# Kernel optimization log

Hardware: AMD Instinct MI355X
Metric: run time of the kernel (lower is better)

## Reference

```python
import jax, jax.numpy as jnp
import numpy as np

# dims: M scalars (0e), K vectors (1e) in input; T = tp_features; N = batch of atoms
M, K, T, N = 128, 64, 64, 131072
D_IN = M + 3 * K  # 320, e3nn layout: [128x0e | 64x1e flattened as (mul, 3)]


def _act_norm(f):
    # e3nn Activation normalizes act so E_{z~N(0,1)}[act(z)^2] = 1
    z = np.linspace(-8.0, 8.0, 20001)
    pdf = np.exp(-0.5 * z * z) / np.sqrt(2.0 * np.pi)
    return float(np.sqrt(np.trapz(f(z) ** 2 * pdf, z)))

C_SILU = _act_norm(lambda z: z / (1.0 + np.exp(-z)))
C_RELU = _act_norm(lambda z: np.maximum(z, 0.0))
INV_SQRT_M = float(1.0 / np.sqrt(M))
INV_SQRT_K = float(1.0 / np.sqrt(K))
INV_SQRT_3 = float(1.0 / np.sqrt(3.0))  # wigner_3j(1,1,0) = delta_ij/sqrt(3)
TP_NORM = float(1.0 / np.sqrt(2.0 * T * T))  # fan-in over the 2 paths into 0e


def setup_inputs() -> dict:
    key = jax.random.key(0)
    ks = jax.random.split(key, 11)
    f32 = jnp.float32
    return {
        "x": jax.random.normal(ks[0], (N, D_IN), f32),
        "input_shift": jnp.zeros((D_IN,), f32),
        "output_scale": jnp.ones((), f32),
        # PerceptronLayer 1: Linear (Mx0e+Kx1e) -> ((M+K)x0e + Kx1e)
        "w0_1": jax.random.normal(ks[1], (M, M + K), f32),
        "b0_1": jnp.zeros((M + K,), f32),
        "w1_1": jax.random.normal(ks[2], (K, K), f32),
        # PerceptronLayer 2 (same irreps, resnet applies)
        "w0_2": jax.random.normal(ks[3], (M, M + K), f32),
        "b0_2": jnp.zeros((M + K,), f32),
        "w1_2": jax.random.normal(ks[4], (K, K), f32),
        # linear_out: (Mx0e+Kx1e) -> (Tx0e+Tx1e)
        "w0_o": jax.random.normal(ks[5], (M, T), f32),
        "b0_o": jnp.zeros((T,), f32),
        "w1_o": jax.random.normal(ks[6], (K, T), f32),
        # FullyConnectedTensorProduct (tp, tp) -> 1x0e: paths 0e*0e->0e, 1e*1e->0e
        "w_tp0": jax.random.normal(ks[7], (T, T), f32),
        "w_tp1": jax.random.normal(ks[8], (T, T), f32),
    }


def _linear(xs, xv, w0, b0, w1):
    # e3nn o3.Linear: per-irrep dense mixing with 1/sqrt(fan_in), bias on 0e only
    ys = xs @ w0 * INV_SQRT_M + b0          # [N, M+K] scalars + gates
    yv = jnp.einsum('nki,kj->nji', xv, w1) * INV_SQRT_K  # [N, K, 3]
    return ys, yv


def _gate(ys, yv):
    # e3nn Gate: silu on 0e scalars, relu on 0e gates, gate the 1e vectors
    s = jax.nn.silu(ys[:, :M]) / C_SILU     # [N, M]
    g = jax.nn.relu(ys[:, M:]) / C_RELU     # [N, K]
    return s, yv * g[:, :, None]


def reference(x, input_shift, output_scale,
              w0_1, b0_1, w1_1, w0_2, b0_2, w1_2,
              w0_o, b0_o, w1_o, w_tp0, w_tp1):
    x = x - input_shift
    xs = x[:, :M]                           # [N, M] 0e block
    xv = x[:, M:].reshape(-1, K, 3)         # [N, K, 3] 1e block
    for (w0, b0, w1) in ((w0_1, b0_1, w1_1), (w0_2, b0_2, w1_2)):
        ys, yv = _linear(xs, xv, w0, b0, w1)
        s, v = _gate(ys, yv)
        xs = xs + s                         # resnet: irreps_in == irreps_out
        xv = xv + v
    # linear_out -> irreps_tp = Tx0e + Tx1e
    zs = xs @ w0_o * INV_SQRT_M + b0_o                    # [N, T]
    zv = jnp.einsum('nki,kj->nji', xv, w1_o) * INV_SQRT_K # [N, T, 3]
    # FullyConnectedTensorProduct(z, z) -> 0e (avoid [N,T,T] blowup)
    y0 = jnp.sum((zs @ w_tp0) * zs, axis=-1)                                    # [N]
    y1 = jnp.sum(jnp.einsum('nui,uv->nvi', zv, w_tp1) * zv, axis=(1, 2)) * INV_SQRT_3
    y = (y0 + y1) * TP_NORM / output_scale
    return y[:, None]
```

## Files before the change

kernel.cpp:

```cpp
#include <hip/hip_runtime.h>
#include <math.h>


typedef _Float16 f16;
typedef _Float16 f16x8 __attribute__((ext_vector_type(8)));
typedef __fp16   fp16x2 __attribute__((ext_vector_type(2)));
typedef float    f32x4 __attribute__((ext_vector_type(4)));
typedef int      i32x4 __attribute__((ext_vector_type(4)));

#define MFMA16(a, b, c) __builtin_amdgcn_mfma_f32_16x16x32_f16(a, b, c, 0, 0, 0)

constexpr float INV_SQRT_M = 0.08838834764831845f;
constexpr float INV_SQRT_K = 0.125f;
constexpr float INV_SQRT_3 = 0.57735026918962576f;
constexpr float TP_NORM    = 0.011048543456039806f;

#define OFF_W01 0
#define OFF_W11 24576
#define OFF_W02 28672
#define OFF_W12 53248
#define OFF_W0O 57344
#define OFF_W1O 65536
#define OFF_TP0 69632
#define OFF_TP1 73728
#define PACK_UNITS 9728
#define FB01 38912
#define FB02 39104
#define FB0O 39296
#define TOTAL_UNITS (PACK_UNITS + 448)

#define LDS_W1     24576
#define LDS_BIAS_F 14336
#define LDS_W0O    0
#define LDS_W1O    8192
#define LDS_TP0    12288
#define LDS_TP1    16384
#define LDS_B0O_F  10240

#define NTHR 512

__global__ void pack_and_consts(const float* __restrict__ w01, const float* __restrict__ w11,
                                const float* __restrict__ w02, const float* __restrict__ w12,
                                const float* __restrict__ w0o, const float* __restrict__ w1o,
                                const float* __restrict__ tp0, const float* __restrict__ tp1,
                                const float* __restrict__ b01, const float* __restrict__ b02,
                                const float* __restrict__ b0o,
                                f16* __restrict__ dst, float* __restrict__ ws) {
    if (blockIdx.x == 40) {
        __shared__ double red[256];
        const int t = threadIdx.x;
        double acc_s = 0.0, acc_r = 0.0;
        for (int i = t; i <= 20000; i += 256) {
            const double z = -8.0 + (16.0 * (double)i) / 20000.0;
            const double pdf = exp(-0.5 * z * z) / 2.5066282746310002;
            const double sil = z / (1.0 + exp(-z));
            const double wgt = (i == 0 || i == 20000) ? 0.5 : 1.0;
            acc_s += wgt * sil * sil * pdf;
            if (z > 0.0) acc_r += wgt * z * z * pdf;
        }
        red[t] = acc_s;
        __syncthreads();
        for (int o = 128; o > 0; o >>= 1) { if (t < o) red[t] += red[t + o]; __syncthreads(); }
        const double tot_s = red[0];
        __syncthreads();
        red[t] = acc_r;
        __syncthreads();
        for (int o = 128; o > 0; o >>= 1) { if (t < o) red[t] += red[t + o]; __syncthreads(); }
        if (t == 0) {
            const double dz = 16.0 / 20000.0;
            ws[0] = (float)(1.0 / sqrt(tot_s * dz));
            ws[1] = (float)(1.0 / sqrt(red[0] * dz));
        }
        return;
    }
    int u = blockIdx.x * 256 + threadIdx.x;
    if (u >= TOTAL_UNITS) return;
    if (u >= PACK_UNITS) {
        const int idx = u - PACK_UNITS;
        float* dstF = (float*)dst;
        if (idx < 192)      dstF[FB01 + idx] = b01[idx];
        else if (idx < 384) dstF[FB02 + (idx - 192)] = b02[idx - 192];
        else                dstF[FB0O + (idx - 384)] = b0o[idx - 384];
        return;
    }
    const float* src; int NC, base, lu = u; float sc;
    if      (lu < 3072) {            src = w01; NC = 192; base = OFF_W01; sc = INV_SQRT_M; }
    else if (lu < 3584) { lu -= 3072; src = w11; NC = 64;  base = OFF_W11; sc = INV_SQRT_K; }
    else if (lu < 6656) { lu -= 3584; src = w02; NC = 192; base = OFF_W02; sc = INV_SQRT_M; }
    else if (lu < 7168) { lu -= 6656; src = w12; NC = 64;  base = OFF_W12; sc = INV_SQRT_K; }
    else if (lu < 8192) { lu -= 7168; src = w0o; NC = 64;  base = OFF_W0O; sc = INV_SQRT_M; }
    else if (lu < 8704) { lu -= 8192; src = w1o; NC = 64;  base = OFF_W1O; sc = INV_SQRT_K; }
    else if (lu < 9216) { lu -= 8704; src = tp0; NC = 64;  base = OFF_TP0; sc = 1.0f; }
    else                { lu -= 9216; src = tp1; NC = 64;  base = OFF_TP1; sc = INV_SQRT_3; }
    const int lane = lu & 63;
    const int frag = lu >> 6;
    const int NT = NC >> 4;
    const int kstep = frag / NT, nj = frag - kstep * NT;
    const int gl  = lane >> 4;
    const int col = nj * 16 + (lane & 15);
    f16 tmp[8];
    #pragma unroll
    for (int e = 0; e < 8; ++e) {
        const int row = kstep * 32 + ((e >> 2) << 4) + (gl << 2) + (e & 3);
        tmp[e] = (f16)(src[(size_t)row * NC + col] * sc);
    }
    *(f16x8*)&dst[(size_t)(base) + (size_t)lu * 8] = *(f16x8*)tmp;
}

__device__ __forceinline__ int pk2i(float a, float b) {
    union { fp16x2 h; int i; } u;
    u.h = __builtin_amdgcn_cvt_pkrtz(a, b);
    return u.i;
}

__device__ __forceinline__ f16x8 packB(f32x4 t0, f32x4 t1) {
    union { i32x4 i; f16x8 v; } u;
    u.i[0] = pk2i(t0[0], t0[1]);
    u.i[1] = pk2i(t0[2], t0[3]);
    u.i[2] = pk2i(t1[0], t1[1]);
    u.i[3] = pk2i(t1[2], t1[3]);
    return u.v;
}

union Frag { f16x8 v; fp16x2 h2[4]; };

__device__ __forceinline__ void resblock32(
    Frag (&xsS)[2][4], Frag (&xvS)[2][3][2],
    const f16* lds, float invCS, float invCR, int l, int g)
{
    const float* biasF = (const float*)lds + LDS_BIAS_F;

    f16x8 xsB[2][4];
    #pragma unroll
    for (int h = 0; h < 2; ++h)
        #pragma unroll
        for (int ks = 0; ks < 4; ++ks)
            xsB[h][ks] = xsS[h][ks].v;

    f16x8 aP[4];
    #pragma unroll
    for (int ks = 0; ks < 4; ++ks)
        aP[ks] = *(const f16x8*)&lds[(size_t)(ks * 12 * 64 + l) * 8];
    f32x4 biasP = *(const f32x4*)&biasF[g * 4];

    float gate[2][4][4];
    #pragma unroll
    for (int nj = 0; nj < 12; ++nj) {
        f16x8 aC[4];
        #pragma unroll
        for (int ks = 0; ks < 4; ++ks) aC[ks] = aP[ks];
        const f32x4 bias = biasP;
        if (nj < 11) {
            #pragma unroll
            for (int ks = 0; ks < 4; ++ks)
                aP[ks] = *(const f16x8*)&lds[(size_t)((ks * 12 + nj + 1) * 64 + l) * 8];
            biasP = *(const f32x4*)&biasF[(nj + 1) * 16 + g * 4];
        }
        f32x4 acc0 = {0.f, 0.f, 0.f, 0.f}, acc1 = {0.f, 0.f, 0.f, 0.f};
        #pragma unroll
        for (int ks = 0; ks < 4; ++ks) {
            acc0 = MFMA16(aC[ks], xsB[0][ks], acc0);
            acc1 = MFMA16(aC[ks], xsB[1][ks], acc1);
        }
        #pragma unroll
        for (int h = 0; h < 2; ++h) {
            const f32x4 acc = h ? acc1 : acc0;
            if (nj < 8) {
                float s[4];
                #pragma unroll
                for (int r = 0; r < 4; ++r) {
                    const float ys = acc[r] + bias[r];
                    s[r] = ys * __builtin_amdgcn_rcpf(1.0f + __expf(-ys)) * invCS;
                }
                xsS[h][nj >> 1].h2[2 * (nj & 1)]     += __builtin_amdgcn_cvt_pkrtz(s[0], s[1]);
                xsS[h][nj >> 1].h2[2 * (nj & 1) + 1] += __builtin_amdgcn_cvt_pkrtz(s[2], s[3]);
            } else {
                #pragma unroll
                for (int r = 0; r < 4; ++r) {
                    const float ys = acc[r] + bias[r];
                    gate[h][nj - 8][r] = fmaxf(ys, 0.f) * invCR;
                }
            }
        }
    }

    #pragma unroll
    for (int i = 0; i < 3; ++i) {
        f32x4 av[2][4];
        #pragma unroll
        for (int nj = 0; nj < 4; ++nj) {
            f32x4 a0 = {0.f, 0.f, 0.f, 0.f}, a1 = {0.f, 0.f, 0.f, 0.f};
            #pragma unroll
            for (int ks = 0; ks < 2; ++ks) {
                const f16x8 a = *(const f16x8*)&lds[LDS_W1 + (size_t)((ks * 4 + nj) * 64 + l) * 8];
                a0 = MFMA16(a, xvS[0][i][ks].v, a0);
                a1 = MFMA16(a, xvS[1][i][ks].v, a1);
            }
            av[0][nj] = a0;
            av[1][nj] = a1;
        }
        #pragma unroll
        for (int nj = 0; nj < 4; ++nj)
            #pragma unroll
            for (int h = 0; h < 2; ++h) {
                float u[4];
                #pragma unroll
                for (int r = 0; r < 4; ++r)
                    u[r] = av[h][nj][r] * gate[h][nj][r];
                xvS[h][i][nj >> 1].h2[2 * (nj & 1)]     += __builtin_amdgcn_cvt_pkrtz(u[0], u[1]);
                xvS[h][i][nj >> 1].h2[2 * (nj & 1) + 1] += __builtin_amdgcn_cvt_pkrtz(u[2], u[3]);
            }
    }
}

__global__ __launch_bounds__(NTHR, 2)
void corrnet_lds(const float* __restrict__ x, const float* __restrict__ shift,
                 const float* __restrict__ oscale,
                 const f16* __restrict__ wp, const float* __restrict__ consts,
                 float* __restrict__ out)
{
    __shared__ __align__(16) f16 smem[29056];
    float* smemF = (float*)smem;
    const float* wpF = (const float*)wp;

    const int t = threadIdx.x;
    const int l = t & 63;
    const int g = l >> 4;
    const int c = l & 15;
    const size_t n0 = (size_t)blockIdx.x * 256 + (size_t)(t >> 6) * 32;

    const float invCS = consts[0], invCR = consts[1];
    const float inv_os = 1.0f / oscale[0];

    #pragma unroll
    for (int it = 0; it < 7; ++it) {
        const int u = it * NTHR + t;
        *(f16x8*)&smem[(size_t)u * 8] = *(const f16x8*)&wp[(size_t)u * 8];
    }
    if (t < 48)
        ((f32x4*)&smemF[LDS_BIAS_F])[t] = ((const f32x4*)&wpF[FB01])[t];

    Frag xsS[2][4];
    Frag xvS[2][3][2];
    #pragma unroll
    for (int h = 0; h < 2; ++h) {
        const float* xrow = x + (n0 + h * 16 + c) * 320;
        #pragma unroll
        for (int ks = 0; ks < 4; ++ks) {
            const int col = ks * 32 + g * 4;
            const f32x4 t0 = *(const f32x4*)(xrow + col)      - *(const f32x4*)(shift + col);
            const f32x4 t1 = *(const f32x4*)(xrow + col + 16) - *(const f32x4*)(shift + col + 16);
            xsS[h][ks].v = packB(t0, t1);
        }
        f32x4 tmp[3][4];
        #pragma unroll
        for (int tau = 0; tau < 4; ++tau) {
            const int col = 128 + 3 * (tau * 16 + g * 4);
            const f32x4 a0 = *(const f32x4*)(xrow + col)     - *(const f32x4*)(shift + col);
            const f32x4 a1 = *(const f32x4*)(xrow + col + 4) - *(const f32x4*)(shift + col + 4);
            const f32x4 a2 = *(const f32x4*)(xrow + col + 8) - *(const f32x4*)(shift + col + 8);
            float arr[12];
            #pragma unroll
            for (int e = 0; e < 4; ++e) {
                arr[e] = a0[e]; arr[4 + e] = a1[e]; arr[8 + e] = a2[e];
            }
            #pragma unroll
            for (int r = 0; r < 4; ++r)
                #pragma unroll
                for (int i = 0; i < 3; ++i)
                    tmp[i][tau][r] = arr[3 * r + i];
        }
        #pragma unroll
        for (int i = 0; i < 3; ++i)
            #pragma unroll
            for (int ks = 0; ks < 2; ++ks)
                xvS[h][i][ks].v = packB(tmp[i][2 * ks], tmp[i][2 * ks + 1]);
    }

    __syncthreads();
    resblock32(xsS, xvS, smem, invCS, invCR, l, g);
    __syncthreads();

    #pragma unroll
    for (int it = 0; it < 7; ++it) {
        const int u = it * NTHR + t;
        *(f16x8*)&smem[(size_t)u * 8] = *(const f16x8*)&wp[(size_t)(OFF_W02) + (size_t)u * 8];
    }
    if (t < 48)
        ((f32x4*)&smemF[LDS_BIAS_F])[t] = ((const f32x4*)&wpF[FB02])[t];
    __syncthreads();
    resblock32(xsS, xvS, smem, invCS, invCR, l, g);
    __syncthreads();

    #pragma unroll
    for (int it = 0; it < 5; ++it) {
        const int u = it * NTHR + t;
        *(f16x8*)&smem[(size_t)u * 8] = *(const f16x8*)&wp[(size_t)(OFF_W0O) + (size_t)u * 8];
    }
    if (t < 16)
        ((f32x4*)&smemF[LDS_B0O_F])[t] = ((const f32x4*)&wpF[FB0O])[t];
    __syncthreads();

    f32x4 zs[2][4];
    #pragma unroll
    for (int nj = 0; nj < 4; ++nj) {
        f32x4 acc0 = {0.f, 0.f, 0.f, 0.f}, acc1 = {0.f, 0.f, 0.f, 0.f};
        #pragma unroll
        for (int ks = 0; ks < 4; ++ks) {
            const f16x8 a = *(const f16x8*)&smem[LDS_W0O + (size_t)((ks * 4 + nj) * 64 + l) * 8];
            acc0 = MFMA16(a, xsS[0][ks].v, acc0);
            acc1 = MFMA16(a, xsS[1][ks].v, acc1);
        }
        const f32x4 bias = *(const f32x4*)&smemF[LDS_B0O_F + nj * 16 + g * 4];
        #pragma unroll
        for (int r = 0; r < 4; ++r) {
            zs[0][nj][r] = acc0[r] + bias[r];
            zs[1][nj][r] = acc1[r] + bias[r];
        }
    }

    float part[2]  = {0.f, 0.f};
    float part1[2] = {0.f, 0.f};

    {
        f16x8 zsB[2][2];
        #pragma unroll
        for (int h = 0; h < 2; ++h)
            #pragma unroll
            for (int ks = 0; ks < 2; ++ks)
                zsB[h][ks] = packB(zs[h][2 * ks], zs[h][2 * ks + 1]);
        #pragma unroll
        for (int nj = 0; nj < 4; ++nj) {
            f32x4 acc0 = {0.f, 0.f, 0.f, 0.f}, acc1 = {0.f, 0.f, 0.f, 0.f};
            #pragma unroll
            for (int ks = 0; ks < 2; ++ks) {
                const f16x8 a = *(const f16x8*)&smem[LDS_TP0 + (size_t)((ks * 4 + nj) * 64 + l) * 8];
                acc0 = MFMA16(a, zsB[0][ks], acc0);
                acc1 = MFMA16(a, zsB[1][ks], acc1);
            }
            #pragma unroll
            for (int r = 0; r < 4; ++r) {
                part[0] += acc0[r] * zs[0][nj][r];
                part[1] += acc1[r] * zs[1][nj][r];
            }
        }
    }

    #pragma unroll
    for (int i = 0; i < 3; ++i) {
        f32x4 zv[2][4];
        #pragma unroll
        for (int nj = 0; nj < 4; ++nj) {
            f32x4 acc0 = {0.f, 0.f, 0.f, 0.f}, acc1 = {0.f, 0.f, 0.f, 0.f};
            #pragma unroll
            for (int ks = 0; ks < 2; ++ks) {
                const f16x8 a = *(const f16x8*)&smem[LDS_W1O + (size_t)((ks * 4 + nj) * 64 + l) * 8];
                acc0 = MFMA16(a, xvS[0][i][ks].v, acc0);
                acc1 = MFMA16(a, xvS[1][i][ks].v, acc1);
            }
            #pragma unroll
            for (int r = 0; r < 4; ++r) {
                zv[0][nj][r] = acc0[r];
                zv[1][nj][r] = acc1[r];
            }
        }
        f16x8 zvB[2][2];
        #pragma unroll
        for (int h = 0; h < 2; ++h)
            #pragma unroll
            for (int ks = 0; ks < 2; ++ks)
                zvB[h][ks] = packB(zv[h][2 * ks], zv[h][2 * ks + 1]);
        #pragma unroll
        for (int nj = 0; nj < 4; ++nj) {
            f32x4 acc0 = {0.f, 0.f, 0.f, 0.f}, acc1 = {0.f, 0.f, 0.f, 0.f};
            #pragma unroll
            for (int ks = 0; ks < 2; ++ks) {
                const f16x8 a = *(const f16x8*)&smem[LDS_TP1 + (size_t)((ks * 4 + nj) * 64 + l) * 8];
                acc0 = MFMA16(a, zvB[0][ks], acc0);
                acc1 = MFMA16(a, zvB[1][ks], acc1);
            }
            #pragma unroll
            for (int r = 0; r < 4; ++r) {
                part1[0] += acc0[r] * zv[0][nj][r];
                part1[1] += acc1[r] * zv[1][nj][r];
            }
        }
    }
    #pragma unroll
    for (int h = 0; h < 2; ++h)
        part[h] += part1[h];

    #pragma unroll
    for (int h = 0; h < 2; ++h) {
        part[h] += __shfl_xor(part[h], 16, 64);
        part[h] += __shfl_xor(part[h], 32, 64);
    }

    if (l < 16)
        out[n0 + l] = part[0] * TP_NORM * inv_os;
    else if (l < 32)
        out[n0 + 16 + (l - 16)] = part[1] * TP_NORM * inv_os;
}

extern "C" void kernel_launch(void* const* d_in, const int* in_sizes, int n_in,
                              void* d_out, int out_size, void* d_ws, size_t ws_size,
                              hipStream_t stream) {
    const float* x      = (const float*)d_in[0];
    const float* shift  = (const float*)d_in[1];
    const float* oscale = (const float*)d_in[2];
    const float* w01    = (const float*)d_in[3];
    const float* b01    = (const float*)d_in[4];
    const float* w11    = (const float*)d_in[5];
    const float* w02    = (const float*)d_in[6];
    const float* b02    = (const float*)d_in[7];
    const float* w12    = (const float*)d_in[8];
    const float* w0o    = (const float*)d_in[9];
    const float* b0o    = (const float*)d_in[10];
    const float* w1o    = (const float*)d_in[11];
    const float* wtp0   = (const float*)d_in[12];
    const float* wtp1   = (const float*)d_in[13];
    float* out    = (float*)d_out;
    float* consts = (float*)d_ws;
    f16*   wp     = (f16*)((char*)d_ws + 16);

    pack_and_consts<<<41, 256, 0, stream>>>(
        w01, w11, w02, w12, w0o, w1o, wtp0, wtp1, b01, b02, b0o, wp, consts);

    const int nblocks = 131072 / 256;
    corrnet_lds<<<nblocks, NTHR, 0, stream>>>(
        x, shift, oscale, wp, consts, out);
}
```

Before: 80.15 us.

## Switch matrix multiplies from 16x16x32 to 32x32x16 MFMA tiles

Replaces every 16x16x32 f16 MFMA with the 32x32x16 variant, so each wave covers its 32 atoms with one 32-wide tile instead of two 16-wide halves. The weight packing, input fragment loading, bias indexing and output reduction are rewritten for the new register layout. The gate activations are now kept as packed half pairs and the vector update multiplies in half precision. The aim is fewer MFMA instructions and fewer LDS weight reads per atom, at the cost of larger accumulators, more register pressure and slightly lower precision in the gating step.

Result: slower. 87.07 us (+8.6%).

```diff
diff --git a/kernel.cpp b/kernel.cpp
--- a/kernel.cpp
+++ b/kernel.cpp
@@ -6,9 +6,10 @@
 typedef _Float16 f16x8 __attribute__((ext_vector_type(8)));
 typedef __fp16   fp16x2 __attribute__((ext_vector_type(2)));
 typedef float    f32x4 __attribute__((ext_vector_type(4)));
+typedef float    f32x16 __attribute__((ext_vector_type(16)));
 typedef int      i32x4 __attribute__((ext_vector_type(4)));
 
-#define MFMA16(a, b, c) __builtin_amdgcn_mfma_f32_16x16x32_f16(a, b, c, 0, 0, 0)
+#define MFMA32(a, b, c) __builtin_amdgcn_mfma_f32_32x32x16_f16(a, b, c, 0, 0, 0)
 
 constexpr float INV_SQRT_M = 0.08838834764831845f;
 constexpr float INV_SQRT_K = 0.125f;
@@ -83,25 +84,24 @@
         else                dstF[FB0O + (idx - 384)] = b0o[idx - 384];
         return;
     }
-    const float* src; int NC, base, lu = u; float sc;
-    if      (lu < 3072) {            src = w01; NC = 192; base = OFF_W01; sc = INV_SQRT_M; }
-    else if (lu < 3584) { lu -= 3072; src = w11; NC = 64;  base = OFF_W11; sc = INV_SQRT_K; }
-    else if (lu < 6656) { lu -= 3584; src = w02; NC = 192; base = OFF_W02; sc = INV_SQRT_M; }
-    else if (lu < 7168) { lu -= 6656; src = w12; NC = 64;  base = OFF_W12; sc = INV_SQRT_K; }
-    else if (lu < 8192) { lu -= 7168; src = w0o; NC = 64;  base = OFF_W0O; sc = INV_SQRT_M; }
-    else if (lu < 8704) { lu -= 8192; src = w1o; NC = 64;  base = OFF_W1O; sc = INV_SQRT_K; }
-    else if (lu < 9216) { lu -= 8704; src = tp0; NC = 64;  base = OFF_TP0; sc = 1.0f; }
-    else                { lu -= 9216; src = tp1; NC = 64;  base = OFF_TP1; sc = INV_SQRT_3; }
+    const float* src; int NC, NSTEP, base, lu = u; float sc;
+    if      (lu < 3072) {            src = w01; NC = 192; NSTEP = 8; base = OFF_W01; sc = INV_SQRT_M; }
+    else if (lu < 3584) { lu -= 3072; src = w11; NC = 64;  NSTEP = 4; base = OFF_W11; sc = INV_SQRT_K; }
+    else if (lu < 6656) { lu -= 3584; src = w02; NC = 192; NSTEP = 8; base = OFF_W02; sc = INV_SQRT_M; }
+    else if (lu < 7168) { lu -= 6656; src = w12; NC = 64;  NSTEP = 4; base = OFF_W12; sc = INV_SQRT_K; }
+    else if (lu < 8192) { lu -= 7168; src = w0o; NC = 64;  NSTEP = 8; base = OFF_W0O; sc = INV_SQRT_M; }
+    else if (lu < 8704) { lu -= 8192; src = w1o; NC = 64;  NSTEP = 4; base = OFF_W1O; sc = INV_SQRT_K; }
+    else if (lu < 9216) { lu -= 8704; src = tp0; NC = 64;  NSTEP = 4; base = OFF_TP0; sc = 1.0f; }
+    else                { lu -= 9216; src = tp1; NC = 64;  NSTEP = 4; base = OFF_TP1; sc = INV_SQRT_3; }
     const int lane = lu & 63;
     const int frag = lu >> 6;
-    const int NT = NC >> 4;
-    const int kstep = frag / NT, nj = frag - kstep * NT;
-    const int gl  = lane >> 4;
-    const int col = nj * 16 + (lane & 15);
+    const int oc = frag / NSTEP, s = frag - oc * NSTEP;
+    const int gl  = lane >> 5;
+    const int col = oc * 32 + (lane & 31);
     f16 tmp[8];
     #pragma unroll
     for (int e = 0; e < 8; ++e) {
-        const int row = kstep * 32 + ((e >> 2) << 4) + (gl << 2) + (e & 3);
+        const int row = s * 16 + (e & 3) + 8 * (e >> 2) + 4 * gl;
         tmp[e] = (f16)(src[(size_t)row * NC + col] * sc);
     }
     *(f16x8*)&dst[(size_t)(base) + (size_t)lu * 8] = *(f16x8*)tmp;
@@ -124,92 +124,80 @@
 
 union Frag { f16x8 v; fp16x2 h2[4]; };
 
-__device__ __forceinline__ void resblock32(
-    Frag (&xsS)[2][4], Frag (&xvS)[2][3][2],
-    const f16* lds, float invCS, float invCR, int l, int g)
+__device__ __forceinline__ f32x16 zero16() {
+    f32x16 z = {0.f,0.f,0.f,0.f,0.f,0.f,0.f,0.f,0.f,0.f,0.f,0.f,0.f,0.f,0.f,0.f};
+    return z;
+}
+
+__device__ __forceinline__ void resblock32x32(
+    Frag (&xsF)[8], Frag (&xvF)[3][4],
+    const f16* lds, float invCS, float invCR, int l, int hi)
 {
     const float* biasF = (const float*)lds + LDS_BIAS_F;
 
-    f16x8 xsB[2][4];
-    #pragma unroll
-    for (int h = 0; h < 2; ++h)
-        #pragma unroll
-        for (int ks = 0; ks < 4; ++ks)
-            xsB[h][ks] = xsS[h][ks].v;
-
-    f16x8 aP[4];
-    #pragma unroll
-    for (int ks = 0; ks < 4; ++ks)
-        aP[ks] = *(const f16x8*)&lds[(size_t)(ks * 12 * 64 + l) * 8];
-    f32x4 biasP = *(const f32x4*)&biasF[g * 4];
-
-    float gate[2][4][4];
-    #pragma unroll
-    for (int nj = 0; nj < 12; ++nj) {
-        f16x8 aC[4];
-        #pragma unroll
-        for (int ks = 0; ks < 4; ++ks) aC[ks] = aP[ks];
-        const f32x4 bias = biasP;
-        if (nj < 11) {
-            #pragma unroll
-            for (int ks = 0; ks < 4; ++ks)
-                aP[ks] = *(const f16x8*)&lds[(size_t)((ks * 12 + nj + 1) * 64 + l) * 8];
-            biasP = *(const f32x4*)&biasF[(nj + 1) * 16 + g * 4];
-        }
-        f32x4 acc0 = {0.f, 0.f, 0.f, 0.f}, acc1 = {0.f, 0.f, 0.f, 0.f};
-        #pragma unroll
-        for (int ks = 0; ks < 4; ++ks) {
-            acc0 = MFMA16(aC[ks], xsB[0][ks], acc0);
-            acc1 = MFMA16(aC[ks], xsB[1][ks], acc1);
-        }
-        #pragma unroll
-        for (int h = 0; h < 2; ++h) {
-            const f32x4 acc = h ? acc1 : acc0;
-            if (nj < 8) {
-                float s[4];
+    f16x8 xsB[8];
+    #pragma unroll
+    for (int s = 0; s < 8; ++s) xsB[s] = xsF[s].v;
+
+    fp16x2 gate[2][8];
+    #pragma unroll
+    for (int oc = 0; oc < 6; ++oc) {
+        f32x16 acc = zero16();
+        #pragma unroll
+        for (int sg = 0; sg < 8; ++sg) {
+            const f16x8 a = *(const f16x8*)&lds[(size_t)((oc * 8 + sg) * 64 + l) * 8];
+            acc = MFMA32(a, xsB[sg], acc);
+        }
+        float ysv[16];
+        #pragma unroll
+        for (int q = 0; q < 4; ++q) {
+            const f32x4 b4 = *(const f32x4*)&biasF[oc * 32 + 8 * q + 4 * hi];
+            #pragma unroll
+            for (int r2 = 0; r2 < 4; ++r2)
+                ysv[4 * q + r2] = acc[4 * q + r2] + b4[r2];
+        }
+        if (oc < 4) {
+            #pragma unroll
+            for (int s = 0; s < 2; ++s)
                 #pragma unroll
-                for (int r = 0; r < 4; ++r) {
-                    const float ys = acc[r] + bias[r];
-                    s[r] = ys * __builtin_amdgcn_rcpf(1.0f + __expf(-ys)) * invCS;
+                for (int d = 0; d < 4; ++d) {
+                    const float y0 = ysv[8 * s + 2 * d], y1 = ysv[8 * s + 2 * d + 1];
+                    const float s0 = y0 * __builtin_amdgcn_rcpf(1.0f + __expf(-y0)) * invCS;
+                    const float s1 = y1 * __builtin_amdgcn_rcpf(1.0f + __expf(-y1)) * invCS;
+                    xsF[2 * oc + s].h2[d] += __builtin_amdgcn_cvt_pkrtz(s0, s1);
                 }
-                xsS[h][nj >> 1].h2[2 * (nj & 1)]     += __builtin_amdgcn_cvt_pkrtz(s[0], s[1]);
-                xsS[h][nj >> 1].h2[2 * (nj & 1) + 1] += __builtin_amdgcn_cvt_pkrtz(s[2], s[3]);
-            } else {
+        } else {
+            #pragma unroll
+            for (int s = 0; s < 2; ++s)
                 #pragma unroll
-                for (int r = 0; r < 4; ++r) {
-                    const float ys = acc[r] + bias[r];
-                    gate[h][nj - 8][r] = fmaxf(ys, 0.f) * invCR;
-                }
-            }
+                for (int d = 0; d < 4; ++d)
+                    gate[oc - 4][4 * s + d] = __builtin_amdgcn_cvt_pkrtz(
+                        fmaxf(ysv[8 * s + 2 * d], 0.f) * invCR,
+                        fmaxf(ysv[8 * s + 2 * d + 1], 0.f) * invCR);
         }
     }
 
     #pragma unroll
     for (int i = 0; i < 3; ++i) {
-        f32x4 av[2][4];
-        #pragma unroll
-        for (int nj = 0; nj < 4; ++nj) {
-            f32x4 a0 = {0.f, 0.f, 0.f, 0.f}, a1 = {0.f, 0.f, 0.f, 0.f};
-            #pragma unroll
-            for (int ks = 0; ks < 2; ++ks) {
-                const f16x8 a = *(const f16x8*)&lds[LDS_W1 + (size_t)((ks * 4 + nj) * 64 + l) * 8];
-                a0 = MFMA16(a, xvS[0][i][ks].v, a0);
-                a1 = MFMA16(a, xvS[1][i][ks].v, a1);
-            }
-            av[0][nj] = a0;
-            av[1][nj] = a1;
-        }
-        #pragma unroll
-        for (int nj = 0; nj < 4; ++nj)
-            #pragma unroll
-            for (int h = 0; h < 2; ++h) {
-                float u[4];
+        f16x8 xvB4[4];
+        #pragma unroll
+        for (int sg = 0; sg < 4; ++sg) xvB4[sg] = xvF[i][sg].v;
+        #pragma unroll
+        for (int oc = 0; oc < 2; ++oc) {
+            f32x16 acc = zero16();
+            #pragma unroll
+            for (int sg = 0; sg < 4; ++sg) {
+                const f16x8 a = *(const f16x8*)&lds[LDS_W1 + (size_t)((oc * 4 + sg) * 64 + l) * 8];
+                acc = MFMA32(a, xvB4[sg], acc);
+            }
+            #pragma unroll
+            for (int s = 0; s < 2; ++s)
                 #pragma unroll
-                for (int r = 0; r < 4; ++r)
-                    u[r] = av[h][nj][r] * gate[h][nj][r];
-                xvS[h][i][nj >> 1].h2[2 * (nj & 1)]     += __builtin_amdgcn_cvt_pkrtz(u[0], u[1]);
-                xvS[h][i][nj >> 1].h2[2 * (nj & 1) + 1] += __builtin_amdgcn_cvt_pkrtz(u[2], u[3]);
-            }
+                for (int d = 0; d < 4; ++d)
+                    xvF[i][2 * oc + s].h2[d] +=
+                        __builtin_amdgcn_cvt_pkrtz(acc[8 * s + 2 * d], acc[8 * s + 2 * d + 1])
+                        * gate[oc][4 * s + d];
+        }
     }
 }
 
@@ -223,10 +211,10 @@
     float* smemF = (float*)smem;
     const float* wpF = (const float*)wp;
 
-    const int t = threadIdx.x;
-    const int l = t & 63;
-    const int g = l >> 4;
-    const int c = l & 15;
+    const int t  = threadIdx.x;
+    const int l  = t & 63;
+    const int hi = l >> 5;
+    const int c  = l & 31;
     const size_t n0 = (size_t)blockIdx.x * 256 + (size_t)(t >> 6) * 32;
 
     const float invCS = consts[0], invCR = consts[1];
@@ -240,45 +228,49 @@
     if (t < 48)
         ((f32x4*)&smemF[LDS_BIAS_F])[t] = ((const f32x4*)&wpF[FB01])[t];
 
-    Frag xsS[2][4];
-    Frag xvS[2][3][2];
-    #pragma unroll
-    for (int h = 0; h < 2; ++h) {
-        const float* xrow = x + (n0 + h * 16 + c) * 320;
-        #pragma unroll
-        for (int ks = 0; ks < 4; ++ks) {
-            const int col = ks * 32 + g * 4;
-            const f32x4 t0 = *(const f32x4*)(xrow + col)      - *(const f32x4*)(shift + col);
-            const f32x4 t1 = *(const f32x4*)(xrow + col + 16) - *(const f32x4*)(shift + col + 16);
-            xsS[h][ks].v = packB(t0, t1);
-        }
-        f32x4 tmp[3][4];
-        #pragma unroll
-        for (int tau = 0; tau < 4; ++tau) {
-            const int col = 128 + 3 * (tau * 16 + g * 4);
-            const f32x4 a0 = *(const f32x4*)(xrow + col)     - *(const f32x4*)(shift + col);
-            const f32x4 a1 = *(const f32x4*)(xrow + col + 4) - *(const f32x4*)(shift + col + 4);
-            const f32x4 a2 = *(const f32x4*)(xrow + col + 8) - *(const f32x4*)(shift + col + 8);
-            float arr[12];
+    Frag xsF[8];
+    Frag xvF[3][4];
+    {
+        const float* xrow = x + (n0 + c) * 320;
+        #pragma unroll
+        for (int G = 0; G < 8; ++G) {
+            const int c0 = 16 * G + 4 * hi;
+            const f32x4 t0 = *(const f32x4*)(xrow + c0)     - *(const f32x4*)(shift + c0);
+            const f32x4 t1 = *(const f32x4*)(xrow + c0 + 8) - *(const f32x4*)(shift + c0 + 8);
+            xsF[G].v = packB(t0, t1);
+        }
+        #pragma unroll
+        for (int G = 0; G < 4; ++G) {
+            const int k0 = 16 * G + 4 * hi;
+            const int p0 = 128 + 3 * k0;
+            const int p1 = 128 + 3 * (k0 + 8);
+            const f32x4 a0 = *(const f32x4*)(xrow + p0)     - *(const f32x4*)(shift + p0);
+            const f32x4 a1 = *(const f32x4*)(xrow + p0 + 4) - *(const f32x4*)(shift + p0 + 4);
+            const f32x4 a2 = *(const f32x4*)(xrow + p0 + 8) - *(const f32x4*)(shift + p0 + 8);
+            const f32x4 b0 = *(const f32x4*)(xrow + p1)     - *(const f32x4*)(shift + p1);
+            const f32x4 b1 = *(const f32x4*)(xrow + p1 + 4) - *(const f32x4*)(shift + p1 + 4);
+            const f32x4 b2 = *(const f32x4*)(xrow + p1 + 8) - *(const f32x4*)(shift + p1 + 8);
+            float ar[12], br[12];
             #pragma unroll
             for (int e = 0; e < 4; ++e) {
-                arr[e] = a0[e]; arr[4 + e] = a1[e]; arr[8 + e] = a2[e];
-            }
-            #pragma unroll
-            for (int r = 0; r < 4; ++r)
+                ar[e] = a0[e]; ar[4 + e] = a1[e]; ar[8 + e] = a2[e];
+                br[e] = b0[e]; br[4 + e] = b1[e]; br[8 + e] = b2[e];
+            }
+            #pragma unroll
+            for (int i = 0; i < 3; ++i) {
+                f32x4 t0, t1;
                 #pragma unroll
-                for (int i = 0; i < 3; ++i)
-                    tmp[i][tau][r] = arr[3 * r + i];
-        }
-        #pragma unroll
-        for (int i = 0; i < 3; ++i)
-            #pragma unroll
-            for (int ks = 0; ks < 2; ++ks)
-                xvS[h][i][ks].v = packB(tmp[i][2 * ks], tmp[i][2 * ks + 1]);
+                for (int j = 0; j < 4; ++j) {
+                    t0[j] = ar[3 * j + i];
+                    t1[j] = br[3 * j + i];
+                }
+                xvF[i][G].v = packB(t0, t1);
+            }
+        }
     }
 
     __syncthreads();
-    resblock32(xsS, xvS, smem, invCS, invCR, l, g);
+    resblock32x32(xsF, xvF, smem, invCS, invCR, l, hi);
     __syncthreads();
 
     #pragma unroll
@@ -289,7 +281,7 @@
     if (t < 48)
         ((f32x4*)&smemF[LDS_BIAS_F])[t] = ((const f32x4*)&wpF[FB02])[t];
     __syncthreads();
-    resblock32(xsS, xvS, smem, invCS, invCR, l, g);
+    resblock32x32(xsF, xvF, smem, invCS, invCR, l, hi);
     __syncthreads();
 
     #pragma unroll
@@ -301,105 +293,91 @@
         ((f32x4*)&smemF[LDS_B0O_F])[t] = ((const f32x4*)&wpF[FB0O])[t];
     __syncthreads();
 
-    f32x4 zs[2][4];
-    #pragma unroll
-    for (int nj = 0; nj < 4; ++nj) {
-        f32x4 acc0 = {0.f, 0.f, 0.f, 0.f}, acc1 = {0.f, 0.f, 0.f, 0.f};
-        #pragma unroll
-        for (int ks = 0; ks < 4; ++ks) {
-            const f16x8 a = *(const f16x8*)&smem[LDS_W0O + (size_t)((ks * 4 + nj) * 64 + l) * 8];
-            acc0 = MFMA16(a, xsS[0][ks].v, acc0);
-            acc1 = MFMA16(a, xsS[1][ks].v, acc1);
-        }
-        const f32x4 bias = *(const f32x4*)&smemF[LDS_B0O_F + nj * 16 + g * 4];
-        #pragma unroll
-        for (int r = 0; r < 4; ++r) {
-            zs[0][nj][r] = acc0[r] + bias[r];
-            zs[1][nj][r] = acc1[r] + bias[r];
-        }
-    }
-
-    float part[2]  = {0.f, 0.f};
-    float part1[2] = {0.f, 0.f};
-
-    {
-        f16x8 zsB[2][2];
-        #pragma unroll
-        for (int h = 0; h < 2; ++h)
-            #pragma unroll
-            for (int ks = 0; ks < 2; ++ks)
-                zsB[h][ks] = packB(zs[h][2 * ks], zs[h][2 * ks + 1]);
-        #pragma unroll
-        for (int nj = 0; nj < 4; ++nj) {
-            f32x4 acc0 = {0.f, 0.f, 0.f, 0.f}, acc1 = {0.f, 0.f, 0.f, 0.f};
-            #pragma unroll
-            for (int ks = 0; ks < 2; ++ks) {
-                const f16x8 a = *(const f16x8*)&smem[LDS_TP0 + (size_t)((ks * 4 + nj) * 64 + l) * 8];
-                acc0 = MFMA16(a, zsB[0][ks], acc0);
-                acc1 = MFMA16(a, zsB[1][ks], acc1);
-            }
-            #pragma unroll
-            for (int r = 0; r < 4; ++r) {
-                part[0] += acc0[r] * zs[0][nj][r];
-                part[1] += acc1[r] * zs[1][nj][r];
-            }
-        }
+    float zsv[2][16];
+    f16x8 zsB[4];
+    #pragma unroll
+    for (int oc = 0; oc < 2; ++oc) {
+        f32x16 acc = zero16();
+        #pragma unroll
+        for (int sg = 0; sg < 8; ++sg) {
+            const f16x8 a = *(const f16x8*)&smem[LDS_W0O + (size_t)((oc * 8 + sg) * 64 + l) * 8];
+            acc = MFMA32(a, xsF[sg].v, acc);
+        }
+        #pragma unroll
+        for (int q = 0; q < 4; ++q) {
+            const f32x4 b4 = *(const f32x4*)&smemF[LDS_B0O_F + oc * 32 + 8 * q + 4 * hi];
+            #pragma unroll
+            for (int r2 = 0; r2 < 4; ++r2)
+                zsv[oc][4 * q + r2] = acc[4 * q + r2] + b4[r2];
+        }
+        #pragma unroll
+        for (int s = 0; s < 2; ++s) {
+            union { i32x4 i; f16x8 v; } u;
+            #pragma unroll
+            for (int d = 0; d < 4; ++d)
+                u.i[d] = pk2i(zsv[oc][8 * s + 2 * d], zsv[oc][8 * s + 2 * d + 1]);
+            zsB[2 * oc + s] = u.v;
+        }
+    }
+
+    float part = 0.f, part1 = 0.f;
+
+    #pragma unroll
+    for (int oc = 0; oc < 2; ++oc) {
+        f32x16 acc = zero16();
+        #pragma unroll
+        for (int sg = 0; sg < 4; ++sg) {
+            const f16x8 a = *(const f16x8*)&smem[LDS_TP0 + (size_t)((oc * 4 + sg) * 64 + l) * 8];
+            acc = MFMA32(a, zsB[sg], acc);
+        }
+        #pragma unroll
+        for (int r = 0; r < 16; ++r)
+            part += acc[r] * zsv[oc][r];
     }
 
     #pragma unroll
     for (int i = 0; i < 3; ++i) {
-        f32x4 zv[2][4];
-        #pragma unroll
-        for (int nj = 0; nj < 4; ++nj) {
-            f32x4 acc0 = {0.f, 0.f, 0.f, 0.f}, acc1 = {0.f, 0.f, 0.f, 0.f};
-            #pragma unroll
-            for (int ks = 0; ks < 2; ++ks) {
-                const f16x8 a = *(const f16x8*)&smem[LDS_W1O + (size_t)((ks * 4 + nj) * 64 + l) * 8];
-                acc0 = MFMA16(a, xvS[0][i][ks].v, acc0);
-                acc1 = MFMA16(a, xvS[1][i][ks].v, acc1);
-            }
-            #pragma unroll
-            for (int r = 0; r < 4; ++r) {
-                zv[0][nj][r] = acc0[r];
-                zv[1][nj][r] = acc1[r];
-            }
-        }
-        f16x8 zvB[2][2];
-        #pragma unroll
-        for (int h = 0; h < 2; ++h)
-            #pragma unroll
-            for (int ks = 0; ks < 2; ++ks)
-                zvB[h][ks] = packB(zv[h][2 * ks], zv[h][2 * ks + 1]);
-        #pragma unroll
-        for (int nj = 0; nj < 4; ++nj) {
-            f32x4 acc0 = {0.f, 0.f, 0.f, 0.f}, acc1 = {0.f, 0.f, 0.f, 0.f};
-            #pragma unroll
-            for (int ks = 0; ks < 2; ++ks) {
-                const f16x8 a = *(const f16x8*)&smem[LDS_TP1 + (size_t)((ks * 4 + nj) * 64 + l) * 8];
-                acc0 = MFMA16(a, zvB[0][ks], acc0);
-                acc1 = MFMA16(a, zvB[1][ks], acc1);
-            }
-            #pragma unroll
-            for (int r = 0; r < 4; ++r) {
-                part1[0] += acc0[r] * zv[0][nj][r];
-                part1[1] += acc1[r] * zv[1][nj][r];
-            }
-        }
-    }
-    #pragma unroll
-    for (int h = 0; h < 2; ++h)
-        part[h] += part1[h];
-
-    #pragma unroll
-    for (int h = 0; h < 2; ++h) {
-        part[h] += __shfl_xor(part[h], 16, 64);
-        part[h] += __shfl_xor(part[h], 32, 64);
-    }
-
-    if (l < 16)
-        out[n0 + l] = part[0] * TP_NORM * inv_os;
-    else if (l < 32)
-        out[n0 + 16 + (l - 16)] = part[1] * TP_NORM * inv_os;
+        float zvv[2][16];
+        f16x8 zvB[4];
+        #pragma unroll
+        for (int oc = 0; oc < 2; ++oc) {
+            f32x16 acc = zero16();
+            #pragma unroll
+            for (int sg = 0; sg < 4; ++sg) {
+                const f16x8 a = *(const f16x8*)&smem[LDS_W1O + (size_t)((oc * 4 + sg) * 64 + l) * 8];
+                acc = MFMA32(a, xvF[i][sg].v, acc);
+            }
+            #pragma unroll
+            for (int r = 0; r < 16; ++r)
+                zvv[oc][r] = acc[r];
+            #pragma unroll
+            for (int s = 0; s < 2; ++s) {
+                union { i32x4 i; f16x8 v; } u;
+                #pragma unroll
+                for (int d = 0; d < 4; ++d)
+                    u.i[d] = pk2i(zvv[oc][8 * s + 2 * d], zvv[oc][8 * s + 2 * d + 1]);
+                zvB[2 * oc + s] = u.v;
+            }
+        }
+        #pragma unroll
+        for (int oc = 0; oc < 2; ++oc) {
+            f32x16 acc = zero16();
+            #pragma unroll
+            for (int sg = 0; sg < 4; ++sg) {
+                const f16x8 a = *(const f16x8*)&smem[LDS_TP1 + (size_t)((oc * 4 + sg) * 64 + l) * 8];
+                acc = MFMA32(a, zvB[sg], acc);
+            }
+            #pragma unroll
+            for (int r = 0; r < 16; ++r)
+                part1 += acc[r] * zvv[oc][r];
+        }
+    }
+    part += part1;
+
+    part += __shfl_xor(part, 32, 64);
+
+    if (l < 32)
+        out[n0 + l] = part * TP_NORM * inv_os;
 }
 
 extern "C" void kernel_launch(void* const* d_in, const int* in_sizes, int n_in,
```
